# Optimization experiments

Hardware: AMD Instinct MI355X
Metric: run time of the kernel (lower is better)

## Reference

```python
import jax, jax.numpy as jnp
import numpy as np

K, C, H, W, B = 128, 128, 24, 8, 32
HW = H * W
EPS = 1e-5


def setup_inputs() -> dict:
    key = jax.random.key(0)
    ks = jax.random.split(key, 4)
    feature = jax.random.normal(ks[0], (B, C, H, W), dtype=jnp.float32)
    target = jax.random.randint(ks[1], (B,), 0, K, dtype=jnp.int64)
    class_memory = jax.random.normal(ks[2], (K, C, H, W), dtype=jnp.float32)
    bn_gamma = jnp.ones((1,), jnp.float32)
    bn_beta = jnp.zeros((1,), jnp.float32)
    fc_w = jax.random.normal(ks[3], (1, 2 * HW), dtype=jnp.float32) / np.sqrt(2 * HW)
    fc_b = jnp.zeros((1,), jnp.float32)
    logit_gamma = jnp.ones((1,), jnp.float32)
    logit_beta = jnp.zeros((1,), jnp.float32)
    return {"feature": feature, "target": target, "class_memory": class_memory,
            "bn_gamma": bn_gamma, "bn_beta": bn_beta, "fc_w": fc_w, "fc_b": fc_b,
            "logit_gamma": logit_gamma, "logit_beta": logit_beta}


def _bn_all(x, gamma, beta):
    # BatchNorm1d with 1 channel in training mode: stats over ALL elements
    mean = x.mean()
    var = ((x - mean) ** 2).mean()  # biased variance, as torch uses for normalization
    return (x - mean) * jax.lax.rsqrt(var + EPS) * gamma[0] + beta[0]


def reference(feature, target, class_memory, bn_gamma, bn_beta, fc_w, fc_b,
              logit_gamma, logit_beta):
    f = feature.reshape(B, C, HW)        # query: [B, C, hw]
    m = class_memory.reshape(K, C, HW)   # memory: [K, C, hw]
    # correlation volume: score[k,b,q,p] = sum_c f[b,c,q] * m[k,c,p]
    corr = jnp.einsum('bcq,kcp->kbqp', f, m)  # [K, B, hw, hw]
    # dual-axis max pooling: best-match over query locs and over memory locs
    score = jnp.concatenate([corr.max(axis=2), corr.max(axis=3)], axis=-1)  # [K,B,2hw]
    score = _bn_all(score, bn_gamma, bn_beta)
    # FC to single logit per (class, sample)
    logits = score.reshape(K * B, 2 * HW) @ fc_w.T + fc_b  # [K*B, 1]
    logits = logits.reshape(K, B).T                         # [B, K]
    logits = _bn_all(logits, logit_gamma, logit_beta)
    # focal binary cross-entropy with logits
    onehot = jax.nn.one_hot(target, K, dtype=logits.dtype)  # [B, K]
    bce = onehot * jax.nn.softplus(-logits) + (1.0 - onehot) * jax.nn.softplus(logits)
    prob = jax.nn.sigmoid(logits)
    weight = jnp.where(onehot > 0.5, 1.0 - prob, prob) ** 2
    loss = (bce * weight).sum(-1)  # [B]
    preds = jnp.argmax(logits, axis=1)
    acc = (preds == target).astype(jnp.float32)
    return loss, acc
```

## Files before the change

kernel.cpp:

```cpp
#include <hip/hip_runtime.h>
#include <math.h>

#define BB 32
#define CCH 128
#define KK 128
#define HWW 192
#define NKB (KK * BB)
#define P2 (2 * HWW)

typedef __attribute__((ext_vector_type(8))) __bf16 bf16x8;
typedef __attribute__((ext_vector_type(16))) float f32x16;

#define A_ELEMS (BB * 8 * 6 * 512)
#define B_ELEMS (KK * 16 * 6 * 512)

__global__ __launch_bounds__(256) void pack_kernel(
    const float* __restrict__ feature,
    const float* __restrict__ class_memory,
    __bf16* __restrict__ A2,
    __bf16* __restrict__ B2,
    unsigned int* __restrict__ counter)
{
    int gid = blockIdx.x * 256 + threadIdx.x;
    if (gid == 0) counter[0] = 0;
    if (gid < 98304) {
        int l = gid & 63;
        int r = gid >> 6;
        int t = r % 6;  r /= 6;
        int ks = r & 7;
        int e = r >> 3;
        const float* src = feature + (size_t)e * CCH * HWW;
        int c0 = ks * 16 + (l >> 5) * 8;
        int q  = t * 32 + (l & 31);
        bf16x8 v;
#pragma unroll
        for (int j = 0; j < 8; ++j) v[j] = (__bf16)src[(c0 + j) * HWW + q];
        *(bf16x8*)(A2 + ((size_t)(e * 8 + ks) * 6 + t) * 512 + l * 8) = v;
    } else {
        int g2 = gid - 98304;
        int l = g2 & 63;
        int r = g2 >> 6;
        int t = r % 6;  r /= 6;
        int ks = r & 7;
        int e = r >> 3;
        const float* src = class_memory + (size_t)e * CCH * HWW;
        int c0 = ks * 16 + (l >> 5) * 8;
        int q  = t * 32 + (l & 31);
        bf16x8 vh, vl;
#pragma unroll
        for (int j = 0; j < 8; ++j) {
            float x = src[(c0 + j) * HWW + q];
            __bf16 h = (__bf16)x;
            vh[j] = h;
            vl[j] = (__bf16)(x - (float)h);
        }
        __bf16* base = B2 + ((size_t)e * 16 + ks) * 3072 + t * 512 + l * 8;
        *(bf16x8*)base = vh;
        *(bf16x8*)(base + 8 * 3072) = vl;
    }
}

__device__ __forceinline__ float softplusf(float x) {
    return fmaxf(x, 0.f) + log1pf(expf(-fabsf(x)));
}

__device__ __forceinline__ float block_sum768(float v, float* tmp) {
    __syncthreads();
    for (int off = 32; off > 0; off >>= 1) v += __shfl_down(v, off);
    if ((threadIdx.x & 63) == 0) tmp[threadIdx.x >> 6] = v;
    __syncthreads();
    float r = 0.f;
#pragma unroll
    for (int i = 0; i < 12; ++i) r += tmp[i];
    return r;
}

#define MFMA32(A, B, C) __builtin_amdgcn_mfma_f32_32x32x16_bf16((A), (B), (C), 0, 0, 0)

__global__ __launch_bounds__(768, 3) void corr_mfma(
    const __bf16* __restrict__ A2,
    const __bf16* __restrict__ B2,
    const float* __restrict__ fc_w,
    float* __restrict__ dot_sw,
    float* __restrict__ psum,
    float* __restrict__ psq,
    unsigned int* __restrict__ counter,
    const float* __restrict__ fc_b,
    const float* __restrict__ bn_gamma,
    const float* __restrict__ bn_beta,
    const float* __restrict__ logit_gamma,
    const float* __restrict__ logit_beta,
    const int* __restrict__ target,
    float* __restrict__ out)
{
    __shared__ __align__(16) __bf16 A_lds[2][8][6][64][8];
    __shared__ __align__(16) __bf16 Blo_lds[8][6][64][8];
    __shared__ float colpart[2][2][192];
    __shared__ float rowpart[2][6][192];
    __shared__ int   lastflag_s;

    const int tid = threadIdx.x;
    const int l   = tid & 63;
    const int lc  = l & 31;
    const int w   = tid >> 6;
    const int wy  = w / 6;
    const int wx  = w % 6;

    const int bid   = blockIdx.x;
    const int xcd   = bid & 7;
    const int slot  = bid >> 3;
    const int k     = xcd * 16 + (slot >> 1);
    const int bhalf = slot & 1;

    const __bf16* bkbase = B2 + (size_t)k * 49152;
    bf16x8 bh[8];
#pragma unroll
    for (int g = 0; g < 8; ++g)
        bh[g] = *(const bf16x8*)(bkbase + g * 3072 + wx * 512 + l * 8);

    float fcw[6];
#pragma unroll
    for (int u = 0; u < 6; ++u) fcw[u] = fc_w[l + 64 * u];

    const int woff  = w * 1024 + l * 16;
    const int wbase = w * 1024;

    auto stageA = [&](int buf2, int b) {
        const char* src = (const char*)A2 + (size_t)b * 49152 + woff;
        char* dst = (char*)&A_lds[buf2][0][0][0][0] + wbase;
#pragma unroll
        for (int i = 0; i < 4; ++i)
            __builtin_amdgcn_global_load_lds(
                (const __attribute__((address_space(1))) void*)(src + i * 12288),
                (__attribute__((address_space(3))) void*)(dst + i * 12288),
                16, 0, 0);
    };
    {
        const char* src = (const char*)B2 + (size_t)k * 98304 + 49152 + woff;
        char* dst = (char*)&Blo_lds[0][0][0][0] + wbase;
#pragma unroll
        for (int i = 0; i < 4; ++i)
            __builtin_amdgcn_global_load_lds(
                (const __attribute__((address_space(1))) void*)(src + i * 12288),
                (__attribute__((address_space(3))) void*)(dst + i * 12288),
                16, 0, 0);
    }
    stageA(0, bhalf * 16);
    __syncthreads();

    for (int bi = 0; bi < 16; ++bi) {
        const int buf = bi & 1;
        const int b   = bhalf * 16 + bi;
        if (bi < 15) stageA(buf ^ 1, b + 1);

        f32x16 acc[3], acc2[3];
#pragma unroll
        for (int i = 0; i < 3; ++i)
#pragma unroll
            for (int rr = 0; rr < 16; ++rr) { acc[i][rr] = 0.f; acc2[i][rr] = 0.f; }

#pragma unroll
        for (int g = 0; g < 8; ++g) {
            bf16x8 a0 = *(const bf16x8*)&A_lds[buf][g][wy * 3 + 0][l][0];
            bf16x8 a1 = *(const bf16x8*)&A_lds[buf][g][wy * 3 + 1][l][0];
            bf16x8 a2 = *(const bf16x8*)&A_lds[buf][g][wy * 3 + 2][l][0];
            bf16x8 bl = *(const bf16x8*)&Blo_lds[g][wx][l][0];
            acc[0]  = MFMA32(a0, bh[g], acc[0]);
            acc[0]  = MFMA32(a0, bl,    acc[0]);
            acc[1]  = MFMA32(a1, bh[g], acc[1]);
            acc[1]  = MFMA32(a1, bl,    acc[1]);
            acc[2]  = MFMA32(a2, bh[g], acc[2]);
            acc[2]  = MFMA32(a2, bl,    acc[2]);
            acc2[0] = MFMA32(bh[g], a0, acc2[0]);
            acc2[0] = MFMA32(bl,    a0, acc2[0]);
            acc2[1] = MFMA32(bh[g], a1, acc2[1]);
            acc2[1] = MFMA32(bl,    a1, acc2[1]);
            acc2[2] = MFMA32(bh[g], a2, acc2[2]);
            acc2[2] = MFMA32(bl,    a2, acc2[2]);
        }

        float cmv = -INFINITY;
#pragma unroll
        for (int i = 0; i < 3; ++i)
#pragma unroll
            for (int rr = 0; rr < 16; ++rr) cmv = fmaxf(cmv, acc[i][rr]);
        cmv = fmaxf(cmv, __shfl_xor(cmv, 32));
        if (l < 32) colpart[buf][wy][wx * 32 + lc] = cmv;

#pragma unroll
        for (int i = 0; i < 3; ++i) {
            float t = -INFINITY;
#pragma unroll
            for (int rr = 0; rr < 16; ++rr) t = fmaxf(t, acc2[i][rr]);
            t = fmaxf(t, __shfl_xor(t, 32));
            if (l < 32) rowpart[buf][wx][(wy * 3 + i) * 32 + lc] = t;
        }

        __syncthreads();

        if (w == 0) {
            float ds = 0.f, s1 = 0.f, s2 = 0.f;
#pragma unroll
            for (int u = 0; u < 3; ++u) {
                int p = l + 64 * u;
                float s = fmaxf(colpart[buf][0][p], colpart[buf][1][p]);
                ds = fmaf(s, fcw[u], ds);
                s1 += s;
                s2 = fmaf(s, s, s2);
            }
#pragma unroll
            for (int u = 0; u < 3; ++u) {
                int q = l + 64 * u;
                float s = rowpart[buf][0][q];
#pragma unroll
                for (int x = 1; x < 6; ++x) s = fmaxf(s, rowpart[buf][x][q]);
                ds = fmaf(s, fcw[3 + u], ds);
                s1 += s;
                s2 = fmaf(s, s, s2);
            }
            for (int off = 32; off > 0; off >>= 1) {
                ds += __shfl_down(ds, off);
                s1 += __shfl_down(s1, off);
                s2 += __shfl_down(s2, off);
            }
            if (l == 0) {
                int kb = k * 32 + b;
                dot_sw[kb] = ds;
                psum[kb]   = s1;
                psq[kb]    = s2;
            }
        }
    }

    __syncthreads();
    if (tid == 0) {
        __threadfence();
        unsigned int old = atomicAdd(counter, 1u);
        lastflag_s = (old == 255u) ? 1 : 0;
    }
    __syncthreads();
    if (!lastflag_s) return;
    __threadfence();

    float* l_s = (float*)&A_lds[0][0][0][0][0];
    float* tmp = l_s + NKB;

    float s1 = 0.f, s2 = 0.f, sw = 0.f;
#pragma unroll
    for (int u = 0; u < 6; ++u) {
        int i = tid + 768 * u;
        if (i < NKB) { s1 += psum[i]; s2 += psq[i]; }
    }
    if (tid < P2) sw = fc_w[tid];

    float S1 = block_sum768(s1, tmp);
    float S2 = block_sum768(s2, tmp);
    float SW = block_sum768(sw, tmp);

    const float N1 = (float)NKB * (float)P2;
    float mean1 = S1 / N1;
    float var1  = S2 / N1 - mean1 * mean1;
    float cA = bn_gamma[0] * rsqrtf(var1 + 1e-5f);
    float cB = (bn_beta[0] - cA * mean1) * SW + fc_b[0];

    float lr[6];
    float t1 = 0.f, t2 = 0.f;
#pragma unroll
    for (int u = 0; u < 6; ++u) {
        int i = tid + 768 * u;
        if (i < NKB) {
            lr[u] = fmaf(cA, dot_sw[i], cB);
            t1 += lr[u];
            t2 = fmaf(lr[u], lr[u], t2);
        } else lr[u] = 0.f;
    }
    float T1 = block_sum768(t1, tmp);
    float T2 = block_sum768(t2, tmp);
    float mean2 = T1 / (float)NKB;
    float var2  = T2 / (float)NKB - mean2 * mean2;
    float cC = logit_gamma[0] * rsqrtf(var2 + 1e-5f);
    float cD = logit_beta[0] - mean2 * cC;

#pragma unroll
    for (int u = 0; u < 6; ++u) {
        int i = tid + 768 * u;
        if (i < NKB) l_s[i] = fmaf(lr[u], cC, cD);
    }
    __syncthreads();

    if (tid < 128) {
        const int b  = tid >> 2;
        const int tt = tid & 3;
        const int tgt = target[b];
        float loss  = 0.f;
        float bestv = -INFINITY;
        int   bestk = 0x7fffffff;
#pragma unroll
        for (int u = 0; u < 32; ++u) {
            int kk = tt + 4 * u;
            float lg = l_s[kk * BB + b];
            float prob = 1.f / (1.f + expf(-lg));
            bool pos = (kk == tgt);
            float wgt = pos ? (1.f - prob) : prob;
            float bce = pos ? softplusf(-lg) : softplusf(lg);
            loss += bce * wgt * wgt;
            if (lg > bestv) { bestv = lg; bestk = kk; }
            else if (lg == bestv && kk < bestk) bestk = kk;
        }
#pragma unroll
        for (int off = 2; off > 0; off >>= 1) {
            loss += __shfl_down(loss, off);
            float ov = __shfl_down(bestv, off);
            int   ok = __shfl_down(bestk, off);
            if (ov > bestv) { bestv = ov; bestk = ok; }
            else if (ov == bestv && ok < bestk) bestk = ok;
        }
        if (tt == 0) {
            out[b]      = loss;
            out[BB + b] = (bestk == tgt) ? 1.f : 0.f;
        }
    }
}

extern "C" void kernel_launch(void* const* d_in, const int* in_sizes, int n_in,
                              void* d_out, int out_size, void* d_ws, size_t ws_size,
                              hipStream_t stream)
{
    const float* feature      = (const float*)d_in[0];
    const int*   target       = (const int*)d_in[1];
    const float* class_memory = (const float*)d_in[2];
    const float* bn_gamma     = (const float*)d_in[3];
    const float* bn_beta      = (const float*)d_in[4];
    const float* fc_w         = (const float*)d_in[5];
    const float* fc_b         = (const float*)d_in[6];
    const float* logit_gamma  = (const float*)d_in[7];
    const float* logit_beta   = (const float*)d_in[8];
    float* out = (float*)d_out;

    __bf16* A2 = (__bf16*)d_ws;
    __bf16* B2 = A2 + A_ELEMS;
    float* dot_sw = (float*)(B2 + B_ELEMS);
    float* psum   = dot_sw + NKB;
    float* psq    = psum + NKB;
    unsigned int* counter = (unsigned int*)(psq + NKB);

    pack_kernel<<<1920, 256, 0, stream>>>(feature, class_memory, A2, B2, counter);
    corr_mfma<<<256, 768, 0, stream>>>(A2, B2, fc_w, dot_sw, psum, psq, counter,
                                       fc_b, bn_gamma, bn_beta,
                                       logit_gamma, logit_beta, target, out);
}
```

Before: 207.7 us.

## Keep B low half in registers and preload A fragments before MFMA loop

The low half of the per-class memory tile now stays in registers (bl[8]) for the whole kernel instead of being staged into LDS, which removes the Blo_lds buffer and its per-iteration LDS reads. All A fragments for the current batch element are read from LDS into registers before the next stage's async copy is issued. The MFMA loop is wrapped in s_setprio to raise wave priority during compute. The trade-off is a large rise in register pressure (an extra 32 registers for bl plus 96 for af) under a launch bound of 768 threads and 3 blocks, which risks spills or lower occupancy.

```diff
diff --git a/kernel.cpp b/kernel.cpp
--- a/kernel.cpp
+++ b/kernel.cpp
@@ -94,7 +94,6 @@
     float* __restrict__ out)
 {
     __shared__ __align__(16) __bf16 A_lds[2][8][6][64][8];
-    __shared__ __align__(16) __bf16 Blo_lds[8][6][64][8];
     __shared__ float colpart[2][2][192];
     __shared__ float rowpart[2][6][192];
     __shared__ int   lastflag_s;
@@ -113,10 +112,12 @@
     const int bhalf = slot & 1;
 
     const __bf16* bkbase = B2 + (size_t)k * 49152;
-    bf16x8 bh[8];
-#pragma unroll
-    for (int g = 0; g < 8; ++g)
+    bf16x8 bh[8], bl[8];
+#pragma unroll
+    for (int g = 0; g < 8; ++g) {
         bh[g] = *(const bf16x8*)(bkbase + g * 3072 + wx * 512 + l * 8);
+        bl[g] = *(const bf16x8*)(bkbase + 24576 + g * 3072 + wx * 512 + l * 8);
+    }
 
     float fcw[6];
 #pragma unroll
@@ -135,22 +136,20 @@
                 (__attribute__((address_space(3))) void*)(dst + i * 12288),
                 16, 0, 0);
     };
-    {
-        const char* src = (const char*)B2 + (size_t)k * 98304 + 49152 + woff;
-        char* dst = (char*)&Blo_lds[0][0][0][0] + wbase;
-#pragma unroll
-        for (int i = 0; i < 4; ++i)
-            __builtin_amdgcn_global_load_lds(
-                (const __attribute__((address_space(1))) void*)(src + i * 12288),
-                (__attribute__((address_space(3))) void*)(dst + i * 12288),
-                16, 0, 0);
-    }
     stageA(0, bhalf * 16);
     __syncthreads();
 
     for (int bi = 0; bi < 16; ++bi) {
         const int buf = bi & 1;
         const int b   = bhalf * 16 + bi;
+
+        bf16x8 af[8][3];
+#pragma unroll
+        for (int g = 0; g < 8; ++g)
+#pragma unroll
+            for (int i = 0; i < 3; ++i)
+                af[g][i] = *(const bf16x8*)&A_lds[buf][g][wy * 3 + i][l][0];
+
         if (bi < 15) stageA(buf ^ 1, b + 1);
 
         f32x16 acc[3], acc2[3];
@@ -159,25 +158,23 @@
 #pragma unroll
             for (int rr = 0; rr < 16; ++rr) { acc[i][rr] = 0.f; acc2[i][rr] = 0.f; }
 
+        __builtin_amdgcn_s_setprio(1);
 #pragma unroll
         for (int g = 0; g < 8; ++g) {
-            bf16x8 a0 = *(const bf16x8*)&A_lds[buf][g][wy * 3 + 0][l][0];
-            bf16x8 a1 = *(const bf16x8*)&A_lds[buf][g][wy * 3 + 1][l][0];
-            bf16x8 a2 = *(const bf16x8*)&A_lds[buf][g][wy * 3 + 2][l][0];
-            bf16x8 bl = *(const bf16x8*)&Blo_lds[g][wx][l][0];
-            acc[0]  = MFMA32(a0, bh[g], acc[0]);
-            acc[0]  = MFMA32(a0, bl,    acc[0]);
-            acc[1]  = MFMA32(a1, bh[g], acc[1]);
-            acc[1]  = MFMA32(a1, bl,    acc[1]);
-            acc[2]  = MFMA32(a2, bh[g], acc[2]);
-            acc[2]  = MFMA32(a2, bl,    acc[2]);
-            acc2[0] = MFMA32(bh[g], a0, acc2[0]);
-            acc2[0] = MFMA32(bl,    a0, acc2[0]);
-            acc2[1] = MFMA32(bh[g], a1, acc2[1]);
-            acc2[1] = MFMA32(bl,    a1, acc2[1]);
-            acc2[2] = MFMA32(bh[g], a2, acc2[2]);
-            acc2[2] = MFMA32(bl,    a2, acc2[2]);
-        }
+            acc[0]  = MFMA32(af[g][0], bh[g], acc[0]);
+            acc[0]  = MFMA32(af[g][0], bl[g], acc[0]);
+            acc[1]  = MFMA32(af[g][1], bh[g], acc[1]);
+            acc[1]  = MFMA32(af[g][1], bl[g], acc[1]);
+            acc[2]  = MFMA32(af[g][2], bh[g], acc[2]);
+            acc[2]  = MFMA32(af[g][2], bl[g], acc[2]);
+            acc2[0] = MFMA32(bh[g], af[g][0], acc2[0]);
+            acc2[0] = MFMA32(bl[g], af[g][0], acc2[0]);
+            acc2[1] = MFMA32(bh[g], af[g][1], acc2[1]);
+            acc2[1] = MFMA32(bl[g], af[g][1], acc2[1]);
+            acc2[2] = MFMA32(bh[g], af[g][2], acc2[2]);
+            acc2[2] = MFMA32(bl[g], af[g][2], acc2[2]);
+        }
+        __builtin_amdgcn_s_setprio(0);
 
         float cmv = -INFINITY;
 #pragma unroll
```

Measured after the change: 434.0 us. +109.0%, slower.

## Fuse pack and correlation kernels into one cooperative launch with grid sync

Applied to the files above, without the earlier changes.

Merges the bf16 packing kernel and the MFMA correlation kernel into a single cooperative kernel that packs in a grid-stride loop, grid-syncs, then computes, and grid-syncs again before block 0 runs the final normalization and loss. It drops one kernel launch and replaces the atomic last-block counter with grid synchronization. The A tile double buffer becomes single-buffered, with the next load issued after the sync, and the score reduction is split across threads through a shared scores array. The cost is two grid-wide barriers, less load/compute overlap, and a lower occupancy hint (2 blocks per CU).

```diff
diff --git a/kernel.cpp b/kernel.cpp
--- a/kernel.cpp
+++ b/kernel.cpp
@@ -1,5 +1,8 @@
 #include <hip/hip_runtime.h>
+#include <hip/hip_cooperative_groups.h>
 #include <math.h>
+
+namespace cg = cooperative_groups;
 
 #define BB 32
 #define CCH 128
@@ -13,52 +16,9 @@
 
 #define A_ELEMS (BB * 8 * 6 * 512)
 #define B_ELEMS (KK * 16 * 6 * 512)
-
-__global__ __launch_bounds__(256) void pack_kernel(
-    const float* __restrict__ feature,
-    const float* __restrict__ class_memory,
-    __bf16* __restrict__ A2,
-    __bf16* __restrict__ B2,
-    unsigned int* __restrict__ counter)
-{
-    int gid = blockIdx.x * 256 + threadIdx.x;
-    if (gid == 0) counter[0] = 0;
-    if (gid < 98304) {
-        int l = gid & 63;
-        int r = gid >> 6;
-        int t = r % 6;  r /= 6;
-        int ks = r & 7;
-        int e = r >> 3;
-        const float* src = feature + (size_t)e * CCH * HWW;
-        int c0 = ks * 16 + (l >> 5) * 8;
-        int q  = t * 32 + (l & 31);
-        bf16x8 v;
-#pragma unroll
-        for (int j = 0; j < 8; ++j) v[j] = (__bf16)src[(c0 + j) * HWW + q];
-        *(bf16x8*)(A2 + ((size_t)(e * 8 + ks) * 6 + t) * 512 + l * 8) = v;
-    } else {
-        int g2 = gid - 98304;
-        int l = g2 & 63;
-        int r = g2 >> 6;
-        int t = r % 6;  r /= 6;
-        int ks = r & 7;
-        int e = r >> 3;
-        const float* src = class_memory + (size_t)e * CCH * HWW;
-        int c0 = ks * 16 + (l >> 5) * 8;
-        int q  = t * 32 + (l & 31);
-        bf16x8 vh, vl;
-#pragma unroll
-        for (int j = 0; j < 8; ++j) {
-            float x = src[(c0 + j) * HWW + q];
-            __bf16 h = (__bf16)x;
-            vh[j] = h;
-            vl[j] = (__bf16)(x - (float)h);
-        }
-        __bf16* base = B2 + ((size_t)e * 16 + ks) * 3072 + t * 512 + l * 8;
-        *(bf16x8*)base = vh;
-        *(bf16x8*)(base + 8 * 3072) = vl;
-    }
-}
+#define PACK_ITEMS (98304 + 393216)
+
+#define MFMA32(A, B, C) __builtin_amdgcn_mfma_f32_32x32x16_bf16((A), (B), (C), 0, 0, 0)
 
 __device__ __forceinline__ float softplusf(float x) {
     return fmaxf(x, 0.f) + log1pf(expf(-fabsf(x)));
@@ -75,174 +35,211 @@
     return r;
 }
 
-#define MFMA32(A, B, C) __builtin_amdgcn_mfma_f32_32x32x16_bf16((A), (B), (C), 0, 0, 0)
-
-__global__ __launch_bounds__(768, 3) void corr_mfma(
-    const __bf16* __restrict__ A2,
-    const __bf16* __restrict__ B2,
+__global__ __launch_bounds__(768, 2) void fused_kernel(
+    const float* __restrict__ feature,
+    const int* __restrict__ target,
+    const float* __restrict__ class_memory,
+    const float* __restrict__ bn_gamma,
+    const float* __restrict__ bn_beta,
     const float* __restrict__ fc_w,
+    const float* __restrict__ fc_b,
+    const float* __restrict__ logit_gamma,
+    const float* __restrict__ logit_beta,
+    __bf16* __restrict__ A2,
+    __bf16* __restrict__ B2,
     float* __restrict__ dot_sw,
     float* __restrict__ psum,
     float* __restrict__ psq,
-    unsigned int* __restrict__ counter,
-    const float* __restrict__ fc_b,
-    const float* __restrict__ bn_gamma,
-    const float* __restrict__ bn_beta,
-    const float* __restrict__ logit_gamma,
-    const float* __restrict__ logit_beta,
-    const int* __restrict__ target,
     float* __restrict__ out)
 {
-    __shared__ __align__(16) __bf16 A_lds[2][8][6][64][8];
+    cg::grid_group grid = cg::this_grid();
+
+    __shared__ __align__(16) __bf16 A_lds[8][6][64][8];
     __shared__ __align__(16) __bf16 Blo_lds[8][6][64][8];
-    __shared__ float colpart[2][2][192];
-    __shared__ float rowpart[2][6][192];
-    __shared__ int   lastflag_s;
+    __shared__ float colpart[2][192];
+    __shared__ float rowpart[6][192];
+    __shared__ float scores[384];
 
     const int tid = threadIdx.x;
-    const int l   = tid & 63;
-    const int lc  = l & 31;
-    const int w   = tid >> 6;
-    const int wy  = w / 6;
-    const int wx  = w % 6;
-
-    const int bid   = blockIdx.x;
-    const int xcd   = bid & 7;
-    const int slot  = bid >> 3;
-    const int k     = xcd * 16 + (slot >> 1);
-    const int bhalf = slot & 1;
-
-    const __bf16* bkbase = B2 + (size_t)k * 49152;
-    bf16x8 bh[8];
-#pragma unroll
-    for (int g = 0; g < 8; ++g)
-        bh[g] = *(const bf16x8*)(bkbase + g * 3072 + wx * 512 + l * 8);
-
-    float fcw[6];
-#pragma unroll
-    for (int u = 0; u < 6; ++u) fcw[u] = fc_w[l + 64 * u];
-
-    const int woff  = w * 1024 + l * 16;
-    const int wbase = w * 1024;
-
-    auto stageA = [&](int buf2, int b) {
-        const char* src = (const char*)A2 + (size_t)b * 49152 + woff;
-        char* dst = (char*)&A_lds[buf2][0][0][0][0] + wbase;
-#pragma unroll
-        for (int i = 0; i < 4; ++i)
-            __builtin_amdgcn_global_load_lds(
-                (const __attribute__((address_space(1))) void*)(src + i * 12288),
-                (__attribute__((address_space(3))) void*)(dst + i * 12288),
-                16, 0, 0);
-    };
+
+    for (int gid = blockIdx.x * 768 + tid; gid < PACK_ITEMS; gid += 256 * 768) {
+        if (gid < 98304) {
+            int l = gid & 63;
+            int r = gid >> 6;
+            int t = r % 6;  r /= 6;
+            int ks = r & 7;
+            int e = r >> 3;
+            const float* src = feature + (size_t)e * CCH * HWW;
+            int c0 = ks * 16 + (l >> 5) * 8;
+            int q  = t * 32 + (l & 31);
+            bf16x8 v;
+#pragma unroll
+            for (int j = 0; j < 8; ++j) v[j] = (__bf16)src[(c0 + j) * HWW + q];
+            *(bf16x8*)(A2 + ((size_t)(e * 8 + ks) * 6 + t) * 512 + l * 8) = v;
+        } else {
+            int g2 = gid - 98304;
+            int l = g2 & 63;
+            int r = g2 >> 6;
+            int t = r % 6;  r /= 6;
+            int ks = r & 7;
+            int e = r >> 3;
+            const float* src = class_memory + (size_t)e * CCH * HWW;
+            int c0 = ks * 16 + (l >> 5) * 8;
+            int q  = t * 32 + (l & 31);
+            bf16x8 vh, vl;
+#pragma unroll
+            for (int j = 0; j < 8; ++j) {
+                float x = src[(c0 + j) * HWW + q];
+                __bf16 h = (__bf16)x;
+                vh[j] = h;
+                vl[j] = (__bf16)(x - (float)h);
+            }
+            __bf16* base = B2 + ((size_t)e * 16 + ks) * 3072 + t * 512 + l * 8;
+            *(bf16x8*)base = vh;
+            *(bf16x8*)(base + 8 * 3072) = vl;
+        }
+    }
+    __threadfence();
+    grid.sync();
+
     {
-        const char* src = (const char*)B2 + (size_t)k * 98304 + 49152 + woff;
-        char* dst = (char*)&Blo_lds[0][0][0][0] + wbase;
-#pragma unroll
-        for (int i = 0; i < 4; ++i)
-            __builtin_amdgcn_global_load_lds(
-                (const __attribute__((address_space(1))) void*)(src + i * 12288),
-                (__attribute__((address_space(3))) void*)(dst + i * 12288),
-                16, 0, 0);
-    }
-    stageA(0, bhalf * 16);
-    __syncthreads();
-
-    for (int bi = 0; bi < 16; ++bi) {
-        const int buf = bi & 1;
-        const int b   = bhalf * 16 + bi;
-        if (bi < 15) stageA(buf ^ 1, b + 1);
-
-        f32x16 acc[3], acc2[3];
-#pragma unroll
-        for (int i = 0; i < 3; ++i)
-#pragma unroll
-            for (int rr = 0; rr < 16; ++rr) { acc[i][rr] = 0.f; acc2[i][rr] = 0.f; }
-
-#pragma unroll
-        for (int g = 0; g < 8; ++g) {
-            bf16x8 a0 = *(const bf16x8*)&A_lds[buf][g][wy * 3 + 0][l][0];
-            bf16x8 a1 = *(const bf16x8*)&A_lds[buf][g][wy * 3 + 1][l][0];
-            bf16x8 a2 = *(const bf16x8*)&A_lds[buf][g][wy * 3 + 2][l][0];
-            bf16x8 bl = *(const bf16x8*)&Blo_lds[g][wx][l][0];
-            acc[0]  = MFMA32(a0, bh[g], acc[0]);
-            acc[0]  = MFMA32(a0, bl,    acc[0]);
-            acc[1]  = MFMA32(a1, bh[g], acc[1]);
-            acc[1]  = MFMA32(a1, bl,    acc[1]);
-            acc[2]  = MFMA32(a2, bh[g], acc[2]);
-            acc[2]  = MFMA32(a2, bl,    acc[2]);
-            acc2[0] = MFMA32(bh[g], a0, acc2[0]);
-            acc2[0] = MFMA32(bl,    a0, acc2[0]);
-            acc2[1] = MFMA32(bh[g], a1, acc2[1]);
-            acc2[1] = MFMA32(bl,    a1, acc2[1]);
-            acc2[2] = MFMA32(bh[g], a2, acc2[2]);
-            acc2[2] = MFMA32(bl,    a2, acc2[2]);
-        }
-
-        float cmv = -INFINITY;
-#pragma unroll
-        for (int i = 0; i < 3; ++i)
-#pragma unroll
-            for (int rr = 0; rr < 16; ++rr) cmv = fmaxf(cmv, acc[i][rr]);
-        cmv = fmaxf(cmv, __shfl_xor(cmv, 32));
-        if (l < 32) colpart[buf][wy][wx * 32 + lc] = cmv;
-
-#pragma unroll
-        for (int i = 0; i < 3; ++i) {
-            float t = -INFINITY;
-#pragma unroll
-            for (int rr = 0; rr < 16; ++rr) t = fmaxf(t, acc2[i][rr]);
-            t = fmaxf(t, __shfl_xor(t, 32));
-            if (l < 32) rowpart[buf][wx][(wy * 3 + i) * 32 + lc] = t;
-        }
-
+        const int l   = tid & 63;
+        const int lc  = l & 31;
+        const int w   = tid >> 6;
+        const int wy  = w / 6;
+        const int wx  = w % 6;
+
+        const int bid   = blockIdx.x;
+        const int xcd   = bid & 7;
+        const int slot  = bid >> 3;
+        const int k     = xcd * 16 + (slot >> 1);
+        const int bhalf = slot & 1;
+
+        const __bf16* bkbase = B2 + (size_t)k * 49152;
+        bf16x8 bh[8];
+#pragma unroll
+        for (int g = 0; g < 8; ++g)
+            bh[g] = *(const bf16x8*)(bkbase + g * 3072 + wx * 512 + l * 8);
+
+        float fcw[6];
+#pragma unroll
+        for (int u = 0; u < 6; ++u) fcw[u] = fc_w[l + 64 * u];
+
+        const int woff  = w * 1024 + l * 16;
+        const int wbase = w * 1024;
+
+        auto stageA = [&](int b) {
+            const char* src = (const char*)A2 + (size_t)b * 49152 + woff;
+            char* dst = (char*)&A_lds[0][0][0][0] + wbase;
+#pragma unroll
+            for (int i = 0; i < 4; ++i)
+                __builtin_amdgcn_global_load_lds(
+                    (const __attribute__((address_space(1))) void*)(src + i * 12288),
+                    (__attribute__((address_space(3))) void*)(dst + i * 12288),
+                    16, 0, 0);
+        };
+        {
+            const char* src = (const char*)B2 + (size_t)k * 98304 + 49152 + woff;
+            char* dst = (char*)&Blo_lds[0][0][0][0] + wbase;
+#pragma unroll
+            for (int i = 0; i < 4; ++i)
+                __builtin_amdgcn_global_load_lds(
+                    (const __attribute__((address_space(1))) void*)(src + i * 12288),
+                    (__attribute__((address_space(3))) void*)(dst + i * 12288),
+                    16, 0, 0);
+        }
+        stageA(bhalf * 16);
         __syncthreads();
 
-        if (w == 0) {
-            float ds = 0.f, s1 = 0.f, s2 = 0.f;
-#pragma unroll
-            for (int u = 0; u < 3; ++u) {
-                int p = l + 64 * u;
-                float s = fmaxf(colpart[buf][0][p], colpart[buf][1][p]);
-                ds = fmaf(s, fcw[u], ds);
-                s1 += s;
-                s2 = fmaf(s, s, s2);
-            }
-#pragma unroll
-            for (int u = 0; u < 3; ++u) {
-                int q = l + 64 * u;
-                float s = rowpart[buf][0][q];
-#pragma unroll
-                for (int x = 1; x < 6; ++x) s = fmaxf(s, rowpart[buf][x][q]);
-                ds = fmaf(s, fcw[3 + u], ds);
-                s1 += s;
-                s2 = fmaf(s, s, s2);
-            }
-            for (int off = 32; off > 0; off >>= 1) {
-                ds += __shfl_down(ds, off);
-                s1 += __shfl_down(s1, off);
-                s2 += __shfl_down(s2, off);
-            }
-            if (l == 0) {
-                int kb = k * 32 + b;
-                dot_sw[kb] = ds;
-                psum[kb]   = s1;
-                psq[kb]    = s2;
-            }
-        }
-    }
-
-    __syncthreads();
-    if (tid == 0) {
-        __threadfence();
-        unsigned int old = atomicAdd(counter, 1u);
-        lastflag_s = (old == 255u) ? 1 : 0;
-    }
-    __syncthreads();
-    if (!lastflag_s) return;
+        for (int bi = 0; bi < 16; ++bi) {
+            const int b = bhalf * 16 + bi;
+
+            f32x16 acc[3], acc2[3];
+#pragma unroll
+            for (int i = 0; i < 3; ++i)
+#pragma unroll
+                for (int rr = 0; rr < 16; ++rr) { acc[i][rr] = 0.f; acc2[i][rr] = 0.f; }
+
+#pragma unroll
+            for (int g = 0; g < 8; ++g) {
+                bf16x8 a0 = *(const bf16x8*)&A_lds[g][wy * 3 + 0][l][0];
+                bf16x8 a1 = *(const bf16x8*)&A_lds[g][wy * 3 + 1][l][0];
+                bf16x8 a2 = *(const bf16x8*)&A_lds[g][wy * 3 + 2][l][0];
+                bf16x8 bl = *(const bf16x8*)&Blo_lds[g][wx][l][0];
+                acc[0]  = MFMA32(a0, bh[g], acc[0]);
+                acc[0]  = MFMA32(a0, bl,    acc[0]);
+                acc[1]  = MFMA32(a1, bh[g], acc[1]);
+                acc[1]  = MFMA32(a1, bl,    acc[1]);
+                acc[2]  = MFMA32(a2, bh[g], acc[2]);
+                acc[2]  = MFMA32(a2, bl,    acc[2]);
+                acc2[0] = MFMA32(bh[g], a0, acc2[0]);
+                acc2[0] = MFMA32(bl,    a0, acc2[0]);
+                acc2[1] = MFMA32(bh[g], a1, acc2[1]);
+                acc2[1] = MFMA32(bl,    a1, acc2[1]);
+                acc2[2] = MFMA32(bh[g], a2, acc2[2]);
+                acc2[2] = MFMA32(bl,    a2, acc2[2]);
+            }
+
+            float cmv = -INFINITY;
+#pragma unroll
+            for (int i = 0; i < 3; ++i)
+#pragma unroll
+                for (int rr = 0; rr < 16; ++rr) cmv = fmaxf(cmv, acc[i][rr]);
+            cmv = fmaxf(cmv, __shfl_xor(cmv, 32));
+            if (l < 32) colpart[wy][wx * 32 + lc] = cmv;
+
+#pragma unroll
+            for (int i = 0; i < 3; ++i) {
+                float t = -INFINITY;
+#pragma unroll
+                for (int rr = 0; rr < 16; ++rr) t = fmaxf(t, acc2[i][rr]);
+                t = fmaxf(t, __shfl_xor(t, 32));
+                if (l < 32) rowpart[wx][(wy * 3 + i) * 32 + lc] = t;
+            }
+            __syncthreads();
+
+            if (bi < 15) stageA(b + 1);
+
+            if (tid < 192) {
+                scores[tid] = fmaxf(colpart[0][tid], colpart[1][tid]);
+            } else if (tid < 384) {
+                int q = tid - 192;
+                float v = rowpart[0][q];
+#pragma unroll
+                for (int x = 1; x < 6; ++x) v = fmaxf(v, rowpart[x][q]);
+                scores[192 + q] = v;
+            }
+            __syncthreads();
+
+            if (tid < 64) {
+                float ds = 0.f, s1 = 0.f, s2 = 0.f;
+#pragma unroll
+                for (int u = 0; u < 6; ++u) {
+                    float s = scores[l + 64 * u];
+                    ds = fmaf(s, fcw[u], ds);
+                    s1 += s;
+                    s2 = fmaf(s, s, s2);
+                }
+                for (int off = 32; off > 0; off >>= 1) {
+                    ds += __shfl_down(ds, off);
+                    s1 += __shfl_down(s1, off);
+                    s2 += __shfl_down(s2, off);
+                }
+                if (tid == 0) {
+                    int kb = k * 32 + b;
+                    dot_sw[kb] = ds;
+                    psum[kb]   = s1;
+                    psq[kb]    = s2;
+                }
+            }
+        }
+    }
+
     __threadfence();
-
-    float* l_s = (float*)&A_lds[0][0][0][0][0];
+    grid.sync();
+    if (blockIdx.x != 0) return;
+
+    float* l_s = (float*)&A_lds[0][0][0][0];
     float* tmp = l_s + NKB;
 
     float s1 = 0.f, s2 = 0.f, sw = 0.f;
@@ -342,10 +339,14 @@
     float* dot_sw = (float*)(B2 + B_ELEMS);
     float* psum   = dot_sw + NKB;
     float* psq    = psum + NKB;
-    unsigned int* counter = (unsigned int*)(psq + NKB);
-
-    pack_kernel<<<1920, 256, 0, stream>>>(feature, class_memory, A2, B2, counter);
-    corr_mfma<<<256, 768, 0, stream>>>(A2, B2, fc_w, dot_sw, psum, psq, counter,
-                                       fc_b, bn_gamma, bn_beta,
-                                       logit_gamma, logit_beta, target, out);
+
+    void* args[] = {
+        (void*)&feature, (void*)&target, (void*)&class_memory,
+        (void*)&bn_gamma, (void*)&bn_beta, (void*)&fc_w, (void*)&fc_b,
+        (void*)&logit_gamma, (void*)&logit_beta,
+        (void*)&A2, (void*)&B2, (void*)&dot_sw, (void*)&psum, (void*)&psq,
+        (void*)&out
+    };
+    hipLaunchCooperativeKernel((const void*)fused_kernel,
+                               dim3(256), dim3(768), args, 0, stream);
 }
```

New measurement: 398.8 us. +92.0%, slower.

## Drop low-part MFMAs for row-max path and restructure per-batch score reduction

Applied to the files above, without the earlier changes.

The transposed accumulator used for the max-over-memory-locations path now uses only the high bf16 part of the memory operand and drops the low-part correction MFMAs. This cuts a quarter of the matrix instructions in the inner loop, at the cost of lower precision on half of the pooled scores. The A-tile prefetch moves to after the MFMA loop, and that loop runs at raised wave priority via s_setprio. The colpart/rowpart buffers are no longer double-buffered, and the cross-wave max reduction is spread over 384 threads into a shared scores array before a single wave does the FC dot and stats. The launch-bounds occupancy hint drops from 3 to 2.

```diff
diff --git a/kernel.cpp b/kernel.cpp
--- a/kernel.cpp
+++ b/kernel.cpp
@@ -77,7 +77,7 @@
 
 #define MFMA32(A, B, C) __builtin_amdgcn_mfma_f32_32x32x16_bf16((A), (B), (C), 0, 0, 0)
 
-__global__ __launch_bounds__(768, 3) void corr_mfma(
+__global__ __launch_bounds__(768, 2) void corr_mfma(
     const __bf16* __restrict__ A2,
     const __bf16* __restrict__ B2,
     const float* __restrict__ fc_w,
@@ -95,8 +95,9 @@
 {
     __shared__ __align__(16) __bf16 A_lds[2][8][6][64][8];
     __shared__ __align__(16) __bf16 Blo_lds[8][6][64][8];
-    __shared__ float colpart[2][2][192];
-    __shared__ float rowpart[2][6][192];
+    __shared__ float colpart[2][192];
+    __shared__ float rowpart[6][192];
+    __shared__ float scores[384];
     __shared__ int   lastflag_s;
 
     const int tid = threadIdx.x;
@@ -151,7 +152,6 @@
     for (int bi = 0; bi < 16; ++bi) {
         const int buf = bi & 1;
         const int b   = bhalf * 16 + bi;
-        if (bi < 15) stageA(buf ^ 1, b + 1);
 
         f32x16 acc[3], acc2[3];
 #pragma unroll
@@ -159,6 +159,7 @@
 #pragma unroll
             for (int rr = 0; rr < 16; ++rr) { acc[i][rr] = 0.f; acc2[i][rr] = 0.f; }
 
+        __builtin_amdgcn_s_setprio(1);
 #pragma unroll
         for (int g = 0; g < 8; ++g) {
             bf16x8 a0 = *(const bf16x8*)&A_lds[buf][g][wy * 3 + 0][l][0];
@@ -172,12 +173,12 @@
             acc[2]  = MFMA32(a2, bh[g], acc[2]);
             acc[2]  = MFMA32(a2, bl,    acc[2]);
             acc2[0] = MFMA32(bh[g], a0, acc2[0]);
-            acc2[0] = MFMA32(bl,    a0, acc2[0]);
             acc2[1] = MFMA32(bh[g], a1, acc2[1]);
-            acc2[1] = MFMA32(bl,    a1, acc2[1]);
             acc2[2] = MFMA32(bh[g], a2, acc2[2]);
-            acc2[2] = MFMA32(bl,    a2, acc2[2]);
-        }
+        }
+        __builtin_amdgcn_s_setprio(0);
+
+        if (bi < 15) stageA(buf ^ 1, b + 1);
 
         float cmv = -INFINITY;
 #pragma unroll
@@ -185,7 +186,7 @@
 #pragma unroll
             for (int rr = 0; rr < 16; ++rr) cmv = fmaxf(cmv, acc[i][rr]);
         cmv = fmaxf(cmv, __shfl_xor(cmv, 32));
-        if (l < 32) colpart[buf][wy][wx * 32 + lc] = cmv;
+        if (l < 32) colpart[wy][wx * 32 + lc] = cmv;
 
 #pragma unroll
         for (int i = 0; i < 3; ++i) {
@@ -193,28 +194,27 @@
 #pragma unroll
             for (int rr = 0; rr < 16; ++rr) t = fmaxf(t, acc2[i][rr]);
             t = fmaxf(t, __shfl_xor(t, 32));
-            if (l < 32) rowpart[buf][wx][(wy * 3 + i) * 32 + lc] = t;
-        }
-
+            if (l < 32) rowpart[wx][(wy * 3 + i) * 32 + lc] = t;
+        }
         __syncthreads();
 
-        if (w == 0) {
+        if (tid < 192) {
+            scores[tid] = fmaxf(colpart[0][tid], colpart[1][tid]);
+        } else if (tid < 384) {
+            int q = tid - 192;
+            float v = rowpart[0][q];
+#pragma unroll
+            for (int x = 1; x < 6; ++x) v = fmaxf(v, rowpart[x][q]);
+            scores[192 + q] = v;
+        }
+        __syncthreads();
+
+        if (tid < 64) {
             float ds = 0.f, s1 = 0.f, s2 = 0.f;
 #pragma unroll
-            for (int u = 0; u < 3; ++u) {
-                int p = l + 64 * u;
-                float s = fmaxf(colpart[buf][0][p], colpart[buf][1][p]);
+            for (int u = 0; u < 6; ++u) {
+                float s = scores[l + 64 * u];
                 ds = fmaf(s, fcw[u], ds);
-                s1 += s;
-                s2 = fmaf(s, s, s2);
-            }
-#pragma unroll
-            for (int u = 0; u < 3; ++u) {
-                int q = l + 64 * u;
-                float s = rowpart[buf][0][q];
-#pragma unroll
-                for (int x = 1; x < 6; ++x) s = fmaxf(s, rowpart[buf][x][q]);
-                ds = fmaf(s, fcw[3 + u], ds);
                 s1 += s;
                 s2 = fmaf(s, s, s2);
             }
@@ -223,7 +223,7 @@
                 s1 += __shfl_down(s1, off);
                 s2 += __shfl_down(s2, off);
             }
-            if (l == 0) {
+            if (tid == 0) {
                 int kb = k * 32 + b;
                 dot_sw[kb] = ds;
                 psum[kb]   = s1;
```

Result: faster. 182.4 us (-12.2%).
